# Kernel optimization log

Measured on AMD Instinct MI355X. Metric: run time of the kernel, lower is better.

## Reference

```python
import jax, jax.numpy as jnp
import numpy as np

TOPK = 2
ALPHA = 32.0
EPS = 1e-20


def setup_inputs() -> dict:
    key = jax.random.key(0)
    ks = jax.random.split(key, 6)
    E, D, R, Q, V = 16, 2048, 16, 2048, 512
    B, S = 2, 2048
    return {
        "hidden_states": jax.random.normal(ks[0], (B, S, D), jnp.float32),
        "router_weight": jax.random.normal(ks[1], (E, D), jnp.float32) * 0.02,
        "q_lora_a": jax.random.normal(ks[2], (E, D, R), jnp.float32) * 0.02,
        "q_lora_b": jax.random.normal(ks[3], (E, R, Q), jnp.float32) * 0.02,
        "v_lora_a": jax.random.normal(ks[4], (E, D, R), jnp.float32) * 0.02,
        "v_lora_b": jax.random.normal(ks[5], (E, R, V), jnp.float32) * 0.02,
    }


def reference(hidden_states, router_weight, q_lora_a, q_lora_b, v_lora_a, v_lora_b):
    E, D, R = q_lora_a.shape
    Qo = q_lora_b.shape[-1]
    Vo = v_lora_b.shape[-1]
    scale = ALPHA / float(R)
    orig_shape = hidden_states.shape[:-1]
    h = hidden_states.reshape(-1, D)  # [n, D]
    n = h.shape[0]

    # router: top-k softmax probs, renormalized over the k selected experts
    logits = jnp.einsum('nd,ed->ne', h, router_weight)
    probs = jax.nn.softmax(logits, axis=-1)
    scores, idx = jax.lax.top_k(probs, TOPK)          # [n, k]
    scores = scores / (scores.sum(-1, keepdims=True) + EPS)

    # per-token expert combine weights c[n, e] = scale * sum_k score_k * 1[idx_k == e]
    c = jnp.zeros((n, E), h.dtype).at[jnp.arange(n)[:, None], idx].add(scores * scale)

    # dense per-expert low-rank projections; weighting by c makes non-selected
    # experts contribute zero -> identical math to gather + einsum + weighted sum.
    q_low = jnp.einsum('nd,edr->ner', h, q_lora_a) * c[..., None]  # [n, E, R]
    v_low = jnp.einsum('nd,edr->ner', h, v_lora_a) * c[..., None]
    q_delta = jnp.einsum('ner,erq->nq', q_low, q_lora_b)
    v_delta = jnp.einsum('ner,erv->nv', v_low, v_lora_b)

    return (q_delta.reshape(*orig_shape, Qo), v_delta.reshape(*orig_shape, Vo))
```

## Files before the change

kernel.cpp:

```cpp
#include <hip/hip_runtime.h>
#include <math.h>

#define DD 2048
#define EE 16
#define RR 16
#define QO 2048
#define VO 512
#define DSPLIT 8
#define DRANGE (DD / DSPLIT)
#define DC 64
#define RDC 256
#define DSPL 8
#define TW 4
#define TBI (TW * 4)
#define ABLK 8
#define T2 32
#define CGQ (QO / 256)
#define CGV (VO / 256)

struct Route { int i0, i1; float w0, w1; };

#define DPPF(x, CTRL) __int_as_float(__builtin_amdgcn_update_dpp( \
        0, __float_as_int(x), (CTRL), 0xF, 0xF, true))
__device__ __forceinline__ float rowsum16(float x) {
    x += DPPF(x, 0x108);
    x += DPPF(x, 0x104);
    x += DPPF(x, 0x102);
    x += DPPF(x, 0x101);
    return x;
}
#define DPPD_STEP(x, CTRL)                                                  \
    {                                                                       \
        int lo_ = __builtin_amdgcn_update_dpp(0, __double2loint(x), (CTRL), \
                                              0xF, 0xF, true);              \
        int hi_ = __builtin_amdgcn_update_dpp(0, __double2hiint(x), (CTRL), \
                                              0xF, 0xF, true);              \
        (x) += __hiloint2double(hi_, lo_);                                  \
    }
__device__ __forceinline__ double rowsum16d(double x) {
    DPPD_STEP(x, 0x108);
    DPPD_STEP(x, 0x104);
    DPPD_STEP(x, 0x102);
    DPPD_STEP(x, 0x101);
    return x;
}

__device__ __forceinline__ int apos(int d, int rq) {
    return d * 16 + ((rq ^ ((d >> 1) & 3)) << 2);
}

__global__ __launch_bounds__(256) void logits_kernel(
    const float* __restrict__ h, const float* __restrict__ rw,
    double* __restrict__ lgp, int* __restrict__ cnt, int n)
{
    __shared__ float hs[8 * RDC];

    if (blockIdx.x == 0 && blockIdx.y == 0 && threadIdx.x < EE)
        cnt[threadIdx.x] = 0;

    int t0 = blockIdx.x * 8;
    int ds = blockIdx.y;
    int d0 = ds * RDC;
    int e  = threadIdx.x >> 4;
    int l  = threadIdx.x & 15;

    for (int i = threadIdx.x; i < 8 * (RDC / 4); i += 256) {
        int t = i >> 6, dq = (i & 63) * 4;
        float4 v = make_float4(0.f, 0.f, 0.f, 0.f);
        if (t0 + t < n)
            v = *(const float4*)&h[(size_t)(t0 + t) * DD + d0 + dq];
        *(float4*)&hs[t * RDC + dq] = v;
    }
    __syncthreads();

    double acc[8];
#pragma unroll
    for (int t = 0; t < 8; ++t) acc[t] = 0.0;

    const float* rwe = rw + e * DD + d0;
#pragma unroll
    for (int g = 0; g < RDC / 64; ++g) {
        int d = g * 64 + l * 4;
        float4 r4 = *(const float4*)&rwe[d];
        double rx = r4.x, ry = r4.y, rz = r4.z, rw4 = r4.w;
#pragma unroll
        for (int t = 0; t < 8; ++t) {
            float4 hv = *(const float4*)&hs[t * RDC + d];
            acc[t] += (double)hv.x * rx + (double)hv.y * ry
                    + (double)hv.z * rz + (double)hv.w * rw4;
        }
    }
#pragma unroll
    for (int t = 0; t < 8; ++t) acc[t] = rowsum16d(acc[t]);
    if (l == 0) {
#pragma unroll
        for (int t = 0; t < 8; ++t) {
            int tok = t0 + t;
            if (tok < n)
                lgp[((size_t)tok * DSPL + ds) * EE + e] = acc[t];
        }
    }
}

__global__ __launch_bounds__(256) void finalize_kernel(
    const double* __restrict__ lgp, Route* __restrict__ route,
    unsigned short* __restrict__ bucket, int* __restrict__ cnt, int n)
{
    int j   = threadIdx.x >> 4;
    int l   = threadIdx.x & 15;
    int tok = blockIdx.x * 16 + j;
    if (tok >= n) return;

    const double* p = lgp + (size_t)tok * (DSPL * EE) + l;
    double s = 0.0;
#pragma unroll
    for (int ds = 0; ds < DSPL; ++ds) s += p[ds * EE];

    double m1 = s; int i1 = l;
#pragma unroll
    for (int off = 8; off; off >>= 1) {
        double om = __shfl_xor(m1, off, 16);
        int    oi = __shfl_xor(i1, off, 16);
        if (om > m1 || (om == m1 && oi < i1)) { m1 = om; i1 = oi; }
    }
    double s2 = (l == i1) ? -1.0e300 : s;
    double m2 = s2; int i2 = l;
#pragma unroll
    for (int off = 8; off; off >>= 1) {
        double om = __shfl_xor(m2, off, 16);
        int    oi = __shfl_xor(i2, off, 16);
        if (om > m2 || (om == m2 && oi < i2)) { m2 = om; i2 = oi; }
    }
    if (l == 0) {
        double ed = exp(m2 - m1);
        double w0 = 2.0 / (1.0 + ed);
        Route rt;
        rt.i0 = i1; rt.i1 = i2;
        rt.w0 = (float)w0;
        rt.w1 = (float)(2.0 - w0);
        route[tok] = rt;
        int p0 = atomicAdd(&cnt[i1], 1);
        bucket[(size_t)i1 * n + p0] = (unsigned short)(tok * 2);
        int p1 = atomicAdd(&cnt[i2], 1);
        bucket[(size_t)i2 * n + p1] = (unsigned short)(tok * 2 + 1);
    }
}

__device__ __forceinline__ void loadh(float (&hv)[4][TW],
        const float* const (&hp)[TW], int d0) {
#pragma unroll
    for (int dd = 0; dd < 4; ++dd)
#pragma unroll
        for (int ti = 0; ti < TW; ++ti)
            hv[dd][ti] = hp[ti][d0 + dd * 16];
}

__device__ __forceinline__ void computeh(float (&accq)[TW][4], float (&accv)[TW][4],
        const float (&hv)[4][TW], const float* aq, const float* av,
        int d0, int s, int rp) {
#pragma unroll
    for (int dd = 0; dd < 4; ++dd) {
        int d = d0 + dd * 16 + s;
        float4 aqv = *(const float4*)&aq[apos(d, rp)];
        float4 avv = *(const float4*)&av[apos(d, rp)];
        const float* ap = &aqv.x;
        const float* vp = &avv.x;
#pragma unroll
        for (int ti = 0; ti < TW; ++ti) {
            float hvv = hv[dd][ti];
#pragma unroll
            for (int ri = 0; ri < 4; ++ri) {
                accq[ti][ri] = fmaf(hvv, ap[ri], accq[ti][ri]);
                accv[ti][ri] = fmaf(hvv, vp[ri], accv[ti][ri]);
            }
        }
    }
}

__global__ __launch_bounds__(256, 2) void a_kernel(
    const float* __restrict__ h, const Route* __restrict__ route,
    const unsigned short* __restrict__ bucket, const int* __restrict__ cnt,
    const float* __restrict__ qa, const float* __restrict__ va,
    float* __restrict__ low, int n)
{
    int e  = blockIdx.x;
    int ds = blockIdx.z;
    int cnt_e = cnt[e];
    if ((int)(blockIdx.y * TBI) >= cnt_e) return;

    __align__(16) __shared__ float aq_s[DRANGE * RR];
    __align__(16) __shared__ float av_s[DRANGE * RR];

    const int dbase = ds * DRANGE;
    const float* qa_e = qa + ((size_t)e * DD + dbase) * RR;
    const float* va_e = va + ((size_t)e * DD + dbase) * RR;

    for (int i = threadIdx.x; i < DRANGE * RR / 4; i += 256) {
        int d = i >> 2, rq = i & 3;
        int dst = apos(d, rq);
        *(float4*)&aq_s[dst] = *(const float4*)&qa_e[(size_t)i * 4];
        *(float4*)&av_s[dst] = *(const float4*)&va_e[(size_t)i * 4];
    }
    __syncthreads();

    int lane = threadIdx.x & 63;
    int w    = threadIdx.x >> 6;
    int s    = lane & 15;
    int rp   = lane >> 4;

    for (int cb = blockIdx.y * TBI; cb < cnt_e; cb += gridDim.y * TBI) {
        int cw = cb + w * TW;
        if (cw >= cnt_e) continue;

        int sl = 0; float wt = 0.f;
        if (lane < TW && cw + lane < cnt_e) {
            sl = bucket[(size_t)e * n + cw + lane];
            Route rt = route[sl >> 1];
            wt = (sl & 1) ? rt.w1 : rt.w0;
        }
        const float* hp[TW];
        int   slots[TW];
        float wts[TW];
#pragma unroll
        for (int ti = 0; ti < TW; ++ti) {
            slots[ti] = __shfl(sl, ti);
            wts[ti]   = __shfl(wt, ti);
            hp[ti]    = h + (size_t)(slots[ti] >> 1) * DD + dbase + s;
        }

        float accq[TW][4], accv[TW][4];
#pragma unroll
        for (int ti = 0; ti < TW; ++ti)
#pragma unroll
            for (int ri = 0; ri < 4; ++ri) { accq[ti][ri] = 0.f; accv[ti][ri] = 0.f; }

        float hvA[4][TW], hvB[4][TW];
        loadh(hvA, hp, 0);
#pragma unroll
        for (int d0 = 0; d0 < DRANGE; d0 += 2 * DC) {
            loadh(hvB, hp, d0 + DC);
            computeh(accq, accv, hvA, aq_s, av_s, d0, s, rp);
            if (d0 + 2 * DC < DRANGE) loadh(hvA, hp, d0 + 2 * DC);
            computeh(accq, accv, hvB, aq_s, av_s, d0 + DC, s, rp);
        }

#pragma unroll
        for (int ti = 0; ti < TW; ++ti)
#pragma unroll
            for (int ri = 0; ri < 4; ++ri) {
                accq[ti][ri] = rowsum16(accq[ti][ri]);
                accv[ti][ri] = rowsum16(accv[ti][ri]);
            }
        if (s == 0) {
#pragma unroll
            for (int ti = 0; ti < TW; ++ti) {
                if (cw + ti < cnt_e) {
                    int   sl2 = slots[ti];
                    float wt2 = wts[ti];
                    size_t base = ((size_t)sl2 * DSPLIT + ds) * 32;
                    float4 q4 = make_float4(accq[ti][0] * wt2, accq[ti][1] * wt2,
                                            accq[ti][2] * wt2, accq[ti][3] * wt2);
                    float4 v4 = make_float4(accv[ti][0] * wt2, accv[ti][1] * wt2,
                                            accv[ti][2] * wt2, accv[ti][3] * wt2);
                    *(float4*)&low[base + rp * 4]      = q4;
                    *(float4*)&low[base + 16 + rp * 4] = v4;
                }
            }
        }
    }
}

__global__ __launch_bounds__(256) void b_kernel(
    const Route* __restrict__ route, const float* __restrict__ low,
    const float* __restrict__ qb, const float* __restrict__ vb,
    float* __restrict__ outq, float* __restrict__ outv, int n)
{
    int t0 = blockIdx.x * T2;
    int cg = blockIdx.y;
    int tid = threadIdx.x;

    __shared__ float acc_s[T2 * 256];
    __shared__ float ls[T2 * 2 * RR];
    __shared__ int   elist[EE * T2];
    __shared__ int   ecnt[EE];
    __shared__ Route rts[T2];

    if (tid < EE) ecnt[tid] = 0;
    if (tid < T2) {
        int tok = t0 + tid;
        if (tok < n) rts[tid] = route[tok];
        else { rts[tid].i0 = -1; rts[tid].i1 = -1; rts[tid].w0 = 0.f; rts[tid].w1 = 0.f; }
    }
    __syncthreads();
    if (tid < T2 * 2) {
        int j = tid >> 1, k = tid & 1;
        int e = k ? rts[j].i1 : rts[j].i0;
        if (e >= 0) {
            int p = atomicAdd(&ecnt[e], 1);
            elist[e * T2 + p] = j * 2 + k;
        }
    }
    int side = (cg >= CGQ) ? 1 : 0;
    {
        int slot = tid >> 2, r4 = (tid & 3) * 4;
        int j = slot >> 1, k = slot & 1;
        int tok = t0 + j;
        float4 v = make_float4(0.f, 0.f, 0.f, 0.f);
        if (tok < n) {
            const float* lp = low + (size_t)(tok * 2 + k) * (DSPLIT * 32) + side * 16 + r4;
            float4 acc4 = make_float4(0.f, 0.f, 0.f, 0.f);
#pragma unroll
            for (int dsp = 0; dsp < DSPLIT; ++dsp) {
                float4 p = *(const float4*)(lp + dsp * 32);
                acc4.x += p.x; acc4.y += p.y; acc4.z += p.z; acc4.w += p.w;
            }
            v = acc4;
        }
        *(float4*)&ls[slot * RR + r4] = v;
    }
#pragma unroll
    for (int j = 0; j < T2; ++j) acc_s[j * 256 + tid] = 0.f;
    __syncthreads();

    const float* bp; float* outp; int W, colbase;
    if (cg < CGQ) { bp = qb; outp = outq; W = QO; colbase = cg * 256; }
    else          { bp = vb; outp = outv; W = VO; colbase = (cg - CGQ) * 256; }
    int col = colbase + tid;

    float bcA[RR], bcB[RR];
    {
        const float* be = bp + col;
#pragma unroll
        for (int r = 0; r < RR; ++r) bcA[r] = be[(size_t)r * W];
    }

#define PROC_E(EI, BC)                                                      \
    {                                                                       \
        int c = ecnt[EI];                                                   \
        for (int ii = 0; ii < c; ++ii) {                                    \
            int sk = elist[(EI) * T2 + ii];                                 \
            const float* lp = &ls[sk * RR];                                 \
            float4 l0 = *(const float4*)(lp);                               \
            float4 l1 = *(const float4*)(lp + 4);                           \
            float4 l2 = *(const float4*)(lp + 8);                           \
            float4 l3 = *(const float4*)(lp + 12);                          \
            float v = 0.f;                                                  \
            v = fmaf(l0.x, BC[0],  v); v = fmaf(l0.y, BC[1],  v);           \
            v = fmaf(l0.z, BC[2],  v); v = fmaf(l0.w, BC[3],  v);           \
            v = fmaf(l1.x, BC[4],  v); v = fmaf(l1.y, BC[5],  v);           \
            v = fmaf(l1.z, BC[6],  v); v = fmaf(l1.w, BC[7],  v);           \
            v = fmaf(l2.x, BC[8],  v); v = fmaf(l2.y, BC[9],  v);           \
            v = fmaf(l2.z, BC[10], v); v = fmaf(l2.w, BC[11], v);           \
            v = fmaf(l3.x, BC[12], v); v = fmaf(l3.y, BC[13], v);           \
            v = fmaf(l3.z, BC[14], v); v = fmaf(l3.w, BC[15], v);           \
            acc_s[(sk >> 1) * 256 + tid] += v;   \
        }                                                                   \
    }

    for (int e = 0; e < EE; e += 2) {
        {
            const float* bn = bp + (size_t)(e + 1) * RR * W + col;
#pragma unroll
            for (int r = 0; r < RR; ++r) bcB[r] = bn[(size_t)r * W];
        }
        PROC_E(e, bcA);
        if (e + 2 < EE) {
            const float* bn = bp + (size_t)(e + 2) * RR * W + col;
#pragma unroll
            for (int r = 0; r < RR; ++r) bcA[r] = bn[(size_t)r * W];
        }
        PROC_E(e + 1, bcB);
    }
#undef PROC_E

#pragma unroll
    for (int j = 0; j < T2; ++j) {
        int tok = t0 + j;
        if (tok < n) outp[(size_t)tok * W + col] = acc_s[j * 256 + tid];
    }
}

extern "C" void kernel_launch(void* const* d_in, const int* in_sizes, int n_in,
                              void* d_out, int out_size, void* d_ws, size_t ws_size,
                              hipStream_t stream) {
    const float* h  = (const float*)d_in[0];
    const float* rw = (const float*)d_in[1];
    const float* qa = (const float*)d_in[2];
    const float* qb = (const float*)d_in[3];
    const float* va = (const float*)d_in[4];
    const float* vb = (const float*)d_in[5];

    int n = in_sizes[0] / DD;
    float* out  = (float*)d_out;
    float* outq = out;
    float* outv = out + (size_t)n * QO;

    char* ws = (char*)d_ws;
    Route* route = (Route*)ws;
    size_t off = ((size_t)n * sizeof(Route) + 255) & ~(size_t)255;
    int* cnt = (int*)(ws + off);
    off = (off + EE * sizeof(int) + 255) & ~(size_t)255;
    unsigned short* bucket = (unsigned short*)(ws + off);
    off = (off + (size_t)EE * n * sizeof(unsigned short) + 255) & ~(size_t)255;
    float* low = (float*)(ws + off);
    double* lgp = (double*)low;

    dim3 g1((n + 7) / 8, DSPL);
    logits_kernel<<<g1, 256, 0, stream>>>(h, rw, lgp, cnt, n);

    finalize_kernel<<<(n + 15) / 16, 256, 0, stream>>>(lgp, route, bucket, cnt, n);

    dim3 g2(EE, ABLK, DSPLIT);
    a_kernel<<<g2, 256, 0, stream>>>(h, route, bucket, cnt, qa, va, low, n);

    dim3 g3((n + T2 - 1) / T2, CGQ + CGV);
    b_kernel<<<g3, 256, 0, stream>>>(route, low, qb, vb, outq, outv, n);
}
```

Baseline: 204.6 us.

## Reduce D-split partials with atomics and double B-stage token tile

The A kernel now accumulates its per-D-split low-rank partials directly into a zeroed per-slot buffer with float atomics, rather than writing eight partial slices. The B kernel then reads one summed vector per slot instead of summing eight. The finalize kernel zeroes the buffer, and the B-stage token tile grows from 32 to 64 tokens per block. This trades partial-buffer traffic for atomic contention and nondeterministic summation order, and the larger tile raises shared-memory use in B.

```diff
diff --git a/kernel.cpp b/kernel.cpp
--- a/kernel.cpp
+++ b/kernel.cpp
@@ -14,7 +14,7 @@
 #define TW 4
 #define TBI (TW * 4)
 #define ABLK 8
-#define T2 32
+#define T2 64
 #define CGQ (QO / 256)
 #define CGV (VO / 256)
 
@@ -104,8 +104,12 @@
 
 __global__ __launch_bounds__(256) void finalize_kernel(
     const double* __restrict__ lgp, Route* __restrict__ route,
-    unsigned short* __restrict__ bucket, int* __restrict__ cnt, int n)
+    unsigned short* __restrict__ bucket, int* __restrict__ cnt,
+    float* __restrict__ lowsum, int n)
 {
+    for (int i = blockIdx.x * 256 + threadIdx.x; i < n * 16; i += gridDim.x * 256)
+        *(float4*)&lowsum[(size_t)i * 4] = make_float4(0.f, 0.f, 0.f, 0.f);
+
     int j   = threadIdx.x >> 4;
     int l   = threadIdx.x & 15;
     int tok = blockIdx.x * 16 + j;
@@ -181,7 +185,7 @@
     const float* __restrict__ h, const Route* __restrict__ route,
     const unsigned short* __restrict__ bucket, const int* __restrict__ cnt,
     const float* __restrict__ qa, const float* __restrict__ va,
-    float* __restrict__ low, int n)
+    float* __restrict__ lowsum, int n)
 {
     int e  = blockIdx.x;
     int ds = blockIdx.z;
@@ -257,13 +261,12 @@
                 if (cw + ti < cnt_e) {
                     int   sl2 = slots[ti];
                     float wt2 = wts[ti];
-                    size_t base = ((size_t)sl2 * DSPLIT + ds) * 32;
-                    float4 q4 = make_float4(accq[ti][0] * wt2, accq[ti][1] * wt2,
-                                            accq[ti][2] * wt2, accq[ti][3] * wt2);
-                    float4 v4 = make_float4(accv[ti][0] * wt2, accv[ti][1] * wt2,
-                                            accv[ti][2] * wt2, accv[ti][3] * wt2);
-                    *(float4*)&low[base + rp * 4]      = q4;
-                    *(float4*)&low[base + 16 + rp * 4] = v4;
+                    float* dst = lowsum + (size_t)sl2 * 32;
+#pragma unroll
+                    for (int ri = 0; ri < 4; ++ri) {
+                        atomicAdd(&dst[rp * 4 + ri],      accq[ti][ri] * wt2);
+                        atomicAdd(&dst[16 + rp * 4 + ri], accv[ti][ri] * wt2);
+                    }
                 }
             }
         }
@@ -271,7 +274,7 @@
 }
 
 __global__ __launch_bounds__(256) void b_kernel(
-    const Route* __restrict__ route, const float* __restrict__ low,
+    const Route* __restrict__ route, const float* __restrict__ lowsum,
     const float* __restrict__ qb, const float* __restrict__ vb,
     float* __restrict__ outq, float* __restrict__ outv, int n)
 {
@@ -301,21 +304,13 @@
         }
     }
     int side = (cg >= CGQ) ? 1 : 0;
-    {
-        int slot = tid >> 2, r4 = (tid & 3) * 4;
-        int j = slot >> 1, k = slot & 1;
+    for (int i = tid; i < T2 * 2 * 4; i += 256) {
+        int slot = i >> 2, r4 = (i & 3) * 4;
+        int j = slot >> 1;
         int tok = t0 + j;
         float4 v = make_float4(0.f, 0.f, 0.f, 0.f);
-        if (tok < n) {
-            const float* lp = low + (size_t)(tok * 2 + k) * (DSPLIT * 32) + side * 16 + r4;
-            float4 acc4 = make_float4(0.f, 0.f, 0.f, 0.f);
-#pragma unroll
-            for (int dsp = 0; dsp < DSPLIT; ++dsp) {
-                float4 p = *(const float4*)(lp + dsp * 32);
-                acc4.x += p.x; acc4.y += p.y; acc4.z += p.z; acc4.w += p.w;
-            }
-            v = acc4;
-        }
+        if (tok < n)
+            v = *(const float4*)&lowsum[(size_t)(t0 * 2 + slot) * 32 + side * 16 + r4];
         *(float4*)&ls[slot * RR + r4] = v;
     }
 #pragma unroll
@@ -402,17 +397,19 @@
     off = (off + EE * sizeof(int) + 255) & ~(size_t)255;
     unsigned short* bucket = (unsigned short*)(ws + off);
     off = (off + (size_t)EE * n * sizeof(unsigned short) + 255) & ~(size_t)255;
-    float* low = (float*)(ws + off);
-    double* lgp = (double*)low;
+    double* lgp = (double*)(ws + off);
+    off = (off + (size_t)n * DSPL * EE * sizeof(double) + 255) & ~(size_t)255;
+    float* lowsum = (float*)(ws + off);
 
     dim3 g1((n + 7) / 8, DSPL);
     logits_kernel<<<g1, 256, 0, stream>>>(h, rw, lgp, cnt, n);
 
-    finalize_kernel<<<(n + 15) / 16, 256, 0, stream>>>(lgp, route, bucket, cnt, n);
+    finalize_kernel<<<(n + 15) / 16, 256, 0, stream>>>(lgp, route, bucket, cnt,
+                                                       lowsum, n);
 
     dim3 g2(EE, ABLK, DSPLIT);
-    a_kernel<<<g2, 256, 0, stream>>>(h, route, bucket, cnt, qa, va, low, n);
+    a_kernel<<<g2, 256, 0, stream>>>(h, route, bucket, cnt, qa, va, lowsum, n);
 
     dim3 g3((n + T2 - 1) / T2, CGQ + CGV);
-    b_kernel<<<g3, 256, 0, stream>>>(route, low, qb, vb, outq, outv, n);
-}
+    b_kernel<<<g3, 256, 0, stream>>>(route, lowsum, qb, vb, outq, outv, n);
+}
```

Result: slower. 241.5 us (+18.1%).
